# Kernel tuning notes

Hardware: AMD Instinct MI355X
Metric: run time of the kernel (lower is better)

The kernel has to match this reference:

```python
import jax, jax.numpy as jnp
import numpy as np

REG_MAX = 16
NUM_CLASSES = 30
IMG_SIZE = 320.0


def make_anchors(strides=(8, 16, 32), feats_shapes=((40, 40), (20, 20), (10, 10))):
    pts = []
    for stride, (h, w) in zip(strides, feats_shapes):
        sx = np.arange(w, dtype=np.float32) + 0.5
        sy = np.arange(h, dtype=np.float32) + 0.5
        gy, gx = np.meshgrid(sy, sx, indexing='ij')
        pts.append(np.stack((gx, gy), -1).reshape(-1, 2) * stride)
    return jnp.asarray(np.concatenate(pts, 0))  # [2100, 2]


def setup_inputs() -> dict:
    key = jax.random.key(0)
    k1, k2, k3, k4 = jax.random.split(key, 4)
    B, M = 128, 50
    pred = jax.random.normal(k1, (B, 4 * REG_MAX + NUM_CLASSES, 2100), dtype=jnp.float32)
    targets_cls = jax.random.randint(k2, (B, M), 0, NUM_CLASSES, dtype=jnp.int32)
    targets_xy = jax.random.uniform(k3, (B, M, 2), dtype=jnp.float32)  # normalized centers
    valid = jax.random.randint(k4, (B, M), 0, 2) > 0  # bool GT-validity mask
    anchors = make_anchors()
    return {"pred": pred, "targets_cls": targets_cls, "targets_xy": targets_xy,
            "valid": valid, "anchors": anchors}


def reference(pred, targets_cls, targets_xy, valid, anchors):
    B = pred.shape[0]
    A = anchors.shape[0]  # 2100
    pred_dist = pred[:, :4 * REG_MAX, :]   # [B, 64, A]
    pred_cls = pred[:, 4 * REG_MAX:, :]    # [B, C, A]

    # --- vectorized nearest-anchor assignment (replaces nested python loops) ---
    centers = targets_xy * IMG_SIZE                               # [B, M, 2]
    dist = jnp.linalg.norm(anchors[None, None, :, :] - centers[:, :, None, :], axis=-1)  # [B, M, A]
    best = jnp.argmin(dist, axis=-1)                              # [B, M]

    b_idx = jnp.broadcast_to(jnp.arange(B)[:, None], best.shape)  # [B, M]
    fg_mask = jnp.zeros((B, A), dtype=bool).at[b_idx, best].max(valid)
    target_cls = jnp.zeros_like(pred_cls).at[b_idx, targets_cls, best].max(
        valid.astype(pred_cls.dtype))

    # --- BCEWithLogits, mean over all elements ---
    loss_cls = jnp.mean(-(target_cls * jax.nn.log_sigmoid(pred_cls)
                          + (1.0 - target_cls) * jax.nn.log_sigmoid(-pred_cls)))

    # --- Huber(delta=1) on pred_dist.mean(dim=1)[fg_mask] vs 1.0, mean over fg ---
    m = pred_dist.mean(axis=1)            # [B, A]
    e = m - 1.0
    huber = jnp.where(jnp.abs(e) <= 1.0, 0.5 * e * e, jnp.abs(e) - 0.5)
    cnt = fg_mask.sum().astype(pred.dtype)
    loss_box = jnp.where(cnt > 0,
                         (huber * fg_mask.astype(pred.dtype)).sum() / jnp.maximum(cnt, 1.0),
                         jnp.zeros((), pred.dtype))
    return (loss_box, loss_cls)
```

## Files before the change

### kernel.cpp

```cpp
#include <hip/hip_runtime.h>
#include <cfloat>
#include <cmath>

#define BB 128
#define MM 50
#define AA 2100
#define NC 30
#define DCH 64
#define CHT 94

__device__ __forceinline__ float softplus_f(float x) {
    return fmaxf(x, 0.0f) + log1pf(expf(-fabsf(x)));
}

__global__ void assign_kernel(const float* __restrict__ txy,
                              const int* __restrict__ tcls,
                              const unsigned char* __restrict__ valid,
                              const float* __restrict__ anchors,
                              unsigned int* __restrict__ mask) {
    int gtid = blockIdx.x * blockDim.x + threadIdx.x;
    int pair = gtid >> 6;
    int lane = gtid & 63;
    if (pair >= BB * MM) return;
    if (!valid[pair]) return;

    float cx = txy[pair * 2 + 0] * 320.0f;
    float cy = txy[pair * 2 + 1] * 320.0f;

    float bd = FLT_MAX;
    int   bi = 0x7fffffff;
    for (int a = lane; a < AA; a += 64) {
        float dx = anchors[2 * a]     - cx;
        float dy = anchors[2 * a + 1] - cy;
        float d = sqrtf(dx * dx + dy * dy);
        if (d < bd) { bd = d; bi = a; }
    }
    for (int off = 32; off > 0; off >>= 1) {
        float od = __shfl_xor(bd, off);
        int   oi = __shfl_xor(bi, off);
        if (od < bd || (od == bd && oi < bi)) { bd = od; bi = oi; }
    }
    if (lane == 0) {
        int b = pair / MM;
        int c = tcls[pair];
        atomicOr(&mask[b * AA + bi], (1u << c) | 0x80000000u);
    }
}

__global__ __launch_bounds__(256)
void loss_kernel(const float* __restrict__ pred,
                 const unsigned int* __restrict__ mask,
                 double* __restrict__ sums,
                 unsigned int* __restrict__ cnt) {
    int idx = blockIdx.x * blockDim.x + threadIdx.x;
    double local_cls = 0.0;
    double local_box = 0.0;
    unsigned int local_fg = 0;

    if (idx < BB * AA) {
        int b = idx / AA;
        int a = idx - b * AA;
        const float* pb = pred + (size_t)b * CHT * AA + a;
        unsigned int mw = mask[idx];

        #pragma unroll
        for (int c = 0; c < NC; ++c) {
            float x = pb[(size_t)(DCH + c) * AA];
            float sp = (mw & (1u << c)) ? softplus_f(-x) : softplus_f(x);
            local_cls += (double)sp;
        }

        if (mw & 0x80000000u) {
            float s = 0.0f;
            #pragma unroll
            for (int ch = 0; ch < DCH; ++ch) s += pb[(size_t)ch * AA];
            float m = s * (1.0f / 64.0f);
            float e = m - 1.0f;
            float ae = fabsf(e);
            float huber = (ae <= 1.0f) ? 0.5f * e * e : ae - 0.5f;
            local_box = (double)huber;
            local_fg = 1;
        }
    }

    for (int off = 32; off > 0; off >>= 1) {
        local_cls += __shfl_down(local_cls, off);
        local_box += __shfl_down(local_box, off);
        local_fg  += __shfl_down(local_fg, off);
    }
    __shared__ double s_cls[4];
    __shared__ double s_box[4];
    __shared__ unsigned int s_fg[4];
    int lane = threadIdx.x & 63;
    int w    = threadIdx.x >> 6;
    if (lane == 0) { s_cls[w] = local_cls; s_box[w] = local_box; s_fg[w] = local_fg; }
    __syncthreads();
    if (threadIdx.x == 0) {
        double tc = s_cls[0] + s_cls[1] + s_cls[2] + s_cls[3];
        double tb = s_box[0] + s_box[1] + s_box[2] + s_box[3];
        unsigned int tf = s_fg[0] + s_fg[1] + s_fg[2] + s_fg[3];
        atomicAdd(&sums[0], tc);
        atomicAdd(&sums[1], tb);
        if (tf) atomicAdd(cnt, tf);
    }
}

__global__ void finalize_kernel(const double* __restrict__ sums,
                                const unsigned int* __restrict__ cnt,
                                float* __restrict__ out) {
    double sum_cls = sums[0];
    double sum_box = sums[1];
    unsigned int c = *cnt;
    out[0] = (c > 0) ? (float)(sum_box / (double)c) : 0.0f;
    out[1] = (float)(sum_cls / (double)((size_t)BB * NC * AA));
}

extern "C" void kernel_launch(void* const* d_in, const int* in_sizes, int n_in,
                              void* d_out, int out_size, void* d_ws, size_t ws_size,
                              hipStream_t stream) {
    const float*         pred    = (const float*)d_in[0];
    const int*           tcls    = (const int*)d_in[1];
    const float*         txy     = (const float*)d_in[2];
    const unsigned char* valid   = (const unsigned char*)d_in[3];
    const float*         anchors = (const float*)d_in[4];

    float* out = (float*)d_out;

    const size_t MASK_BYTES = (size_t)BB * AA * sizeof(unsigned int);
    unsigned int* mask = (unsigned int*)d_ws;
    double*       sums = (double*)((char*)d_ws + MASK_BYTES);
    unsigned int* cnt  = (unsigned int*)((char*)d_ws + MASK_BYTES + 2 * sizeof(double));

    hipMemsetAsync(d_ws, 0, MASK_BYTES + 2 * sizeof(double) + sizeof(unsigned int), stream);

    {
        int waves = BB * MM;
        int threads = waves * 64;
        int block = 256;
        int grid = (threads + block - 1) / block;
        assign_kernel<<<grid, block, 0, stream>>>(txy, tcls, valid, anchors, mask);
    }

    {
        int total = BB * AA;
        int block = 256;
        int grid = (total + block - 1) / block;
        loss_kernel<<<grid, block, 0, stream>>>(pred, mask, sums, cnt);
    }

    finalize_kernel<<<1, 1, 0, stream>>>(sums, cnt, out);
}
```

Before: 208.4 us.

## Use float accumulation and fast math in loss kernel, drop sqrt in assignment

The loss kernel now accumulates in float instead of double and swaps log1pf/expf for __logf/__expf. It computes softplus once per element using the identity softplus(-x) = softplus(x) - x, preloads all class logits up front, and counts foreground with a ballot/popcount. The assignment kernel compares squared distances with vectorized float2 anchor loads and an unrolled loop. Together these cut FP64 and transcendental cost, at the risk of small precision differences in the float sums and intrinsics, and possible tie-breaking differences from using squared distance.

```diff
diff --git a/kernel.cpp b/kernel.cpp
--- a/kernel.cpp
+++ b/kernel.cpp
@@ -8,10 +8,6 @@
 #define NC 30
 #define DCH 64
 #define CHT 94
-
-__device__ __forceinline__ float softplus_f(float x) {
-    return fmaxf(x, 0.0f) + log1pf(expf(-fabsf(x)));
-}
 
 __global__ void assign_kernel(const float* __restrict__ txy,
                               const int* __restrict__ tcls,
@@ -27,12 +23,15 @@
     float cx = txy[pair * 2 + 0] * 320.0f;
     float cy = txy[pair * 2 + 1] * 320.0f;
 
+    const float2* __restrict__ anc = (const float2*)anchors;
     float bd = FLT_MAX;
     int   bi = 0x7fffffff;
+    #pragma unroll 4
     for (int a = lane; a < AA; a += 64) {
-        float dx = anchors[2 * a]     - cx;
-        float dy = anchors[2 * a + 1] - cy;
-        float d = sqrtf(dx * dx + dy * dy);
+        float2 p = anc[a];
+        float dx = p.x - cx;
+        float dy = p.y - cy;
+        float d = dx * dx + dy * dy;
         if (d < bd) { bd = d; bi = a; }
     }
     for (int off = 32; off > 0; off >>= 1) {
@@ -53,51 +52,61 @@
                  double* __restrict__ sums,
                  unsigned int* __restrict__ cnt) {
     int idx = blockIdx.x * blockDim.x + threadIdx.x;
-    double local_cls = 0.0;
-    double local_box = 0.0;
-    unsigned int local_fg = 0;
+    float acc_cls = 0.0f;
+    float box = 0.0f;
+    int is_fg = 0;
 
     if (idx < BB * AA) {
         int b = idx / AA;
         int a = idx - b * AA;
-        const float* pb = pred + (size_t)b * CHT * AA + a;
+        const float* __restrict__ pc = pred + (size_t)b * CHT * AA
+                                            + (size_t)DCH * AA + a;
         unsigned int mw = mask[idx];
+
+        float x[NC];
+        #pragma unroll
+        for (int c = 0; c < NC; ++c) x[c] = pc[(size_t)c * AA];
 
         #pragma unroll
         for (int c = 0; c < NC; ++c) {
-            float x = pb[(size_t)(DCH + c) * AA];
-            float sp = (mw & (1u << c)) ? softplus_f(-x) : softplus_f(x);
-            local_cls += (double)sp;
+            float v = x[c];
+            float sp = fmaxf(v, 0.0f) + __logf(1.0f + __expf(-fabsf(v)));
+            acc_cls += sp - (((mw >> c) & 1u) ? v : 0.0f);
         }
 
         if (mw & 0x80000000u) {
+            const float* __restrict__ pd = pred + (size_t)b * CHT * AA + a;
             float s = 0.0f;
-            #pragma unroll
-            for (int ch = 0; ch < DCH; ++ch) s += pb[(size_t)ch * AA];
+            #pragma unroll 16
+            for (int ch = 0; ch < DCH; ++ch) s += pd[(size_t)ch * AA];
             float m = s * (1.0f / 64.0f);
             float e = m - 1.0f;
             float ae = fabsf(e);
-            float huber = (ae <= 1.0f) ? 0.5f * e * e : ae - 0.5f;
-            local_box = (double)huber;
-            local_fg = 1;
+            box = (ae <= 1.0f) ? 0.5f * e * e : ae - 0.5f;
+            is_fg = 1;
         }
     }
 
     for (int off = 32; off > 0; off >>= 1) {
-        local_cls += __shfl_down(local_cls, off);
-        local_box += __shfl_down(local_box, off);
-        local_fg  += __shfl_down(local_fg, off);
+        acc_cls += __shfl_down(acc_cls, off);
+        box     += __shfl_down(box, off);
     }
-    __shared__ double s_cls[4];
-    __shared__ double s_box[4];
+    unsigned long long bal = __ballot(is_fg);
+
+    __shared__ float s_cls[4];
+    __shared__ float s_box[4];
     __shared__ unsigned int s_fg[4];
     int lane = threadIdx.x & 63;
     int w    = threadIdx.x >> 6;
-    if (lane == 0) { s_cls[w] = local_cls; s_box[w] = local_box; s_fg[w] = local_fg; }
+    if (lane == 0) {
+        s_cls[w] = acc_cls;
+        s_box[w] = box;
+        s_fg[w]  = (unsigned int)__popcll(bal);
+    }
     __syncthreads();
     if (threadIdx.x == 0) {
-        double tc = s_cls[0] + s_cls[1] + s_cls[2] + s_cls[3];
-        double tb = s_box[0] + s_box[1] + s_box[2] + s_box[3];
+        double tc = (double)s_cls[0] + s_cls[1] + s_cls[2] + s_cls[3];
+        double tb = (double)s_box[0] + s_box[1] + s_box[2] + s_box[3];
         unsigned int tf = s_fg[0] + s_fg[1] + s_fg[2] + s_fg[3];
         atomicAdd(&sums[0], tc);
         atomicAdd(&sums[1], tb);
@@ -134,19 +143,16 @@
     hipMemsetAsync(d_ws, 0, MASK_BYTES + 2 * sizeof(double) + sizeof(unsigned int), stream);
 
     {
-        int waves = BB * MM;
-        int threads = waves * 64;
+        int threads = BB * MM * 64;
         int block = 256;
         int grid = (threads + block - 1) / block;
         assign_kernel<<<grid, block, 0, stream>>>(txy, tcls, valid, anchors, mask);
     }
-
     {
         int total = BB * AA;
         int block = 256;
         int grid = (total + block - 1) / block;
         loss_kernel<<<grid, block, 0, stream>>>(pred, mask, sums, cnt);
     }
-
     finalize_kernel<<<1, 1, 0, stream>>>(sums, cnt, out);
 }
```

After: 176.2 us. -15.5%, faster.
